# Kernel tuning notes

Hardware: AMD Instinct MI355X
Metric: run time of the kernel (lower is better)

## Reference

```python
import jax, jax.numpy as jnp
import numpy as np

B, S, D, E, TOP_K = 4, 4096, 2048, 64, 2

def setup_inputs() -> dict:
    key = jax.random.key(0)
    k1, k2, k3, k4 = jax.random.split(key, 4)
    return {
        "mh_output": jax.random.normal(k1, (B, S, D), dtype=jnp.float32),
        "W_route": jax.random.normal(k2, (D, E), dtype=jnp.float32) * (1.0 / np.sqrt(D)),
        "b_route": jnp.zeros((E,), dtype=jnp.float32),
        "W_noise": jax.random.normal(k3, (D, E), dtype=jnp.float32) * (1.0 / np.sqrt(D)),
        "b_noise": jnp.zeros((E,), dtype=jnp.float32),
        "noise": jax.random.normal(k4, (B, S, E), dtype=jnp.float32),
    }

def reference(mh_output, W_route, b_route, W_noise, b_noise, noise):
    # logits / noise logits: [B, S, E]
    logits = jnp.einsum("bsd,de->bse", mh_output, W_route) + b_route
    noise_logits = jnp.einsum("bsd,de->bse", mh_output, W_noise) + b_noise
    noisy_logits = logits + noise * jax.nn.softplus(noise_logits)

    top_vals, indices = jax.lax.top_k(noisy_logits, TOP_K)  # [B,S,K]

    # scatter top-k values into a -inf-filled tensor, then softmax
    flat_vals = top_vals.reshape(-1, TOP_K)
    flat_idx = indices.reshape(-1, TOP_K)
    n_tok = flat_idx.shape[0]
    rows = jnp.arange(n_tok)[:, None]
    sparse = jnp.full((n_tok, E), -jnp.inf, dtype=noisy_logits.dtype)
    sparse = sparse.at[rows, flat_idx].set(flat_vals)
    probs = jax.nn.softmax(sparse, axis=-1).reshape(noisy_logits.shape)
    return probs, indices
```

## Files before the change

kernel.cpp:

```cpp
#include <hip/hip_runtime.h>
#include <math.h>

#define M_TOK 16384
#define D_DIM 2048
#define E_EXP 64
#define BM    32
#define NT_H  16
#define FRAG_B 1040
#define TILE_B (12 * FRAG_B)
#define LL_LD 132
#define SMEM_BYTES (4 * TILE_B)

typedef float         f32x16 __attribute__((ext_vector_type(16)));
typedef short         bf16x8 __attribute__((ext_vector_type(8)));
typedef unsigned int  uint;

#define MFMA32(a, b, c) __builtin_amdgcn_mfma_f32_32x32x16_bf16((a), (b), (c), 0, 0, 0)

__device__ __forceinline__ unsigned short bfrne(float f) {
    unsigned int u = __float_as_uint(f);
    return (unsigned short)((u + 0x7fffu + ((u >> 16) & 1u)) >> 16);
}
__device__ __forceinline__ float bfhi(unsigned short h) {
    return __uint_as_float((unsigned int)h << 16);
}

__device__ __forceinline__ bool beats(float va, int ia, float vb, int ib) {
    return (va > vb) || (va == vb && ia < ib);
}

__device__ __forceinline__ void block_sync_lds() {
    asm volatile("s_waitcnt lgkmcnt(0)" ::: "memory");
    __builtin_amdgcn_s_barrier();
    asm volatile("" ::: "memory");
}

__global__ __launch_bounds__(256) void prep_w(
    const float* __restrict__ Wr, const float* __restrict__ Wn,
    unsigned short* __restrict__ Wg)
{
    const int g     = blockIdx.x * 256 + threadIdx.x;
    const int lane  = g & 63;
    const int ch    = (g >> 6) & 3;
    const int kstep = g >> 8;
    const int col   = ch * 32 + (lane & 31);
    const float* __restrict__ W = (col < 64) ? Wr : Wn;
    const int colL  = col & 63;
    const int kbase = kstep * 16 + (lane >> 5) * 8;

    bf16x8 o0, o1, o2;
    #pragma unroll
    for (int j = 0; j < 8; ++j) {
        const float w = W[(size_t)(kbase + j) * E_EXP + colL];
        const unsigned short h0 = bfrne(w);
        const float r  = w - bfhi(h0);
        const unsigned short h1 = bfrne(r);
        const float r2 = r - bfhi(h1);
        const unsigned short h2 = bfrne(r2);
        o0[j] = (short)h0; o1[j] = (short)h1; o2[j] = (short)h2;
    }
    #pragma unroll
    for (int p = 0; p < 3; ++p) {
        const size_t idx = (((size_t)kstep * 3 + p) * 4 + ch) * 64 + lane;
        const bf16x8 o = (p == 0) ? o0 : (p == 1) ? o1 : o2;
        *(bf16x8*)(Wg + idx * 8) = o;
    }
}

__device__ __forceinline__ void load_b_half(const unsigned short* __restrict__ Wg,
                                            int t, int s0, int wc, int lane,
                                            bf16x8 (&Bv)[2][3])
{
    #pragma unroll
    for (int s = 0; s < 2; ++s) {
        const int kstep = t * 4 + s0 + s;
        #pragma unroll
        for (int p = 0; p < 3; ++p) {
            const size_t idx = (((size_t)kstep * 3 + p) * 4 + wc);
            Bv[s][p] = *(const bf16x8*)(Wg + (idx << 9) + lane * 8);
        }
    }
}

__device__ __forceinline__ void load_a(const float* __restrict__ A, int tokBase,
                                       int t, int tid, float4& x)
{
    const int row = tid >> 4;
    const int kc  = tid & 15;
    x = *(const float4*)(A + (size_t)(tokBase + row) * D_DIM + t * 64 + kc * 4);
}

__device__ __forceinline__ void cvt_store(char* tbase, int tid, const float4& x)
{
    const float v[4] = {x.x, x.y, x.z, x.w};
    uint t0[4], t1[4]; unsigned short h2[4];
    #pragma unroll
    for (int j = 0; j < 4; ++j) {
        const uint u = __float_as_uint(v[j]);
        t0[j] = u & 0xffff0000u;
        const float r = v[j] - __uint_as_float(t0[j]);
        const uint ru = __float_as_uint(r);
        t1[j] = ru & 0xffff0000u;
        const float r2 = r - __uint_as_float(t1[j]);
        h2[j] = bfrne(r2);
    }
    uint2 w0, w1, w2;
    w0.x = (t0[0] >> 16) | t0[1];  w0.y = (t0[2] >> 16) | t0[3];
    w1.x = (t1[0] >> 16) | t1[1];  w1.y = (t1[2] >> 16) | t1[3];
    w2.x = (uint)h2[0] | ((uint)h2[1] << 16);
    w2.y = (uint)h2[2] | ((uint)h2[3] << 16);

    const int row   = tid >> 4;
    const int kc    = tid & 15;
    const int kstep = kc >> 2;
    const int hoct  = (kc >> 1) & 1;
    const int half  = kc & 1;
    const int l     = hoct * 32 + row;
    char* p = tbase + kstep * (3 * FRAG_B) + l * 16 + half * 8;
    *(uint2*)(p)              = w0;
    *(uint2*)(p + FRAG_B)     = w1;
    *(uint2*)(p + 2 * FRAG_B) = w2;
}

__device__ __forceinline__ void compute_half(const char* buf, int s0, int lane,
                                             const bf16x8 (&Bv)[2][3],
                                             f32x16& acch, f32x16& accl)
{
    const char* ap = buf + lane * 16;
    #pragma unroll
    for (int s = 0; s < 2; ++s) {
        const int f = (s0 + s) * 3;
        const bf16x8 a0 = *(const bf16x8*)(ap + (f + 0) * FRAG_B);
        const bf16x8 a1 = *(const bf16x8*)(ap + (f + 1) * FRAG_B);
        const bf16x8 a2 = *(const bf16x8*)(ap + (f + 2) * FRAG_B);
        acch = MFMA32(a0, Bv[s][0], acch);
        accl = MFMA32(a0, Bv[s][1], accl);
        accl = MFMA32(a1, Bv[s][0], accl);
        accl = MFMA32(a1, Bv[s][1], accl);
        accl = MFMA32(a0, Bv[s][2], accl);
        accl = MFMA32(a2, Bv[s][0], accl);
    }
}

__global__ __launch_bounds__(512, 4) void fused_router(
    const float* __restrict__ A,
    const unsigned short* __restrict__ Wg,
    const float* __restrict__ br, const float* __restrict__ bn,
    const float* __restrict__ noise,
    float* __restrict__ probs, float* __restrict__ idxo)
{
    __shared__ __align__(16) char smem[SMEM_BYTES];

    const int tid  = threadIdx.x;
    const int lane = tid & 63;
    const int wid  = tid >> 6;
    const int wc   = wid & 3;
    const int kh   = wid >> 2;
    const int tokBase = blockIdx.x * BM;

    f32x16 acch, accl;
    #pragma unroll
    for (int r = 0; r < 16; ++r) { acch[r] = 0.f; accl[r] = 0.f; }

    char* s0a = smem;
    char* s0b = smem + TILE_B;
    char* s1a = smem + 2 * TILE_B;
    char* s1b = smem + 3 * TILE_B;
    const char* myB0 = smem + (kh * 2 + 0) * TILE_B;
    const char* myB1 = smem + (kh * 2 + 1) * TILE_B;

    bf16x8 Bx[2][3], By[2][3];
    float4 x0, x1;

    load_a(A, tokBase, 0,        tid, x0);
    load_a(A, tokBase, NT_H,     tid, x1);
    cvt_store(s0a, tid, x0);
    cvt_store(s1a, tid, x1);
    load_a(A, tokBase, 1,        tid, x0);
    load_a(A, tokBase, NT_H + 1, tid, x1);
    load_b_half(Wg, kh * NT_H, 0, wc, lane, Bx);
    block_sync_lds();

    #pragma unroll 1
    for (int it = 0; it < NT_H; it += 2) {
        const int tA = kh * NT_H + it;

        cvt_store(s0b, tid, x0);
        cvt_store(s1b, tid, x1);
        if (it + 2 < NT_H) {
            load_a(A, tokBase, it + 2,        tid, x0);
            load_a(A, tokBase, NT_H + it + 2, tid, x1);
        }
        load_b_half(Wg, tA, 2, wc, lane, By);
        __builtin_amdgcn_s_setprio(1);
        compute_half(myB0, 0, lane, Bx, acch, accl);
        __builtin_amdgcn_s_setprio(0);
        load_b_half(Wg, tA + 1, 0, wc, lane, Bx);
        __builtin_amdgcn_s_setprio(1);
        compute_half(myB0, 2, lane, By, acch, accl);
        __builtin_amdgcn_s_setprio(0);
        block_sync_lds();

        if (it + 2 < NT_H) {
            cvt_store(s0a, tid, x0);
            cvt_store(s1a, tid, x1);
        }
        if (it + 3 < NT_H) {
            load_a(A, tokBase, it + 3,        tid, x0);
            load_a(A, tokBase, NT_H + it + 3, tid, x1);
        }
        load_b_half(Wg, tA + 1, 2, wc, lane, By);
        __builtin_amdgcn_s_setprio(1);
        compute_half(myB1, 0, lane, Bx, acch, accl);
        __builtin_amdgcn_s_setprio(0);
        if (it + 2 < NT_H) load_b_half(Wg, tA + 2, 0, wc, lane, Bx);
        __builtin_amdgcn_s_setprio(1);
        compute_half(myB1, 2, lane, By, acch, accl);
        __builtin_amdgcn_s_setprio(0);
        block_sync_lds();
    }

    float (*Ll)[BM][LL_LD] = (float (*)[BM][LL_LD])smem;
    {
        const int col   = wc * 32 + (lane & 31);
        const int rbase = 4 * (lane >> 5);
        #pragma unroll
        for (int r = 0; r < 16; ++r) {
            const int row = (r & 3) + 8 * (r >> 2) + rbase;
            Ll[kh][row][col] = acch[r] + accl[r];
        }
    }
    block_sync_lds();

    const int token = tid >> 4;
    const int s16   = tid & 15;
    const int tokG  = tokBase + token;

    float v0 = -INFINITY, v1 = -INFINITY;
    int i0 = 0, i1 = 0;
    {
        const float4 n4 = *(const float4*)(noise + (size_t)tokG * E_EXP + s16 * 4);
        const float4 b4 = *(const float4*)(br + s16 * 4);
        const float4 c4 = *(const float4*)(bn + s16 * 4);
        const float4 la = *(const float4*)(&Ll[0][token][s16 * 4]);
        const float4 lb = *(const float4*)(&Ll[1][token][s16 * 4]);
        const float4 ma = *(const float4*)(&Ll[0][token][64 + s16 * 4]);
        const float4 mb = *(const float4*)(&Ll[1][token][64 + s16 * 4]);
        const float nv[4] = {n4.x, n4.y, n4.z, n4.w};
        const float bv[4] = {b4.x, b4.y, b4.z, b4.w};
        const float cv[4] = {c4.x, c4.y, c4.z, c4.w};
        const float lv[4] = {la.x + lb.x, la.y + lb.y, la.z + lb.z, la.w + lb.w};
        const float mv[4] = {ma.x + mb.x, ma.y + mb.y, ma.z + mb.z, ma.w + mb.w};
        #pragma unroll
        for (int j = 0; j < 4; ++j) {
            const int e = s16 * 4 + j;
            const float lg = lv[j] + bv[j];
            const float nl = mv[j] + cv[j];
            const float sp = fmaxf(nl, 0.0f) + log1pf(expf(-fabsf(nl)));
            const float v  = fmaf(nv[j], sp, lg);
            if (beats(v, e, v0, i0))      { v1 = v0; i1 = i0; v0 = v; i0 = e; }
            else if (beats(v, e, v1, i1)) { v1 = v;  i1 = e; }
        }
    }
    #pragma unroll
    for (int m = 1; m < 16; m <<= 1) {
        const float w0 = __shfl_xor(v0, m), w1 = __shfl_xor(v1, m);
        const int   j0 = __shfl_xor(i0, m), j1 = __shfl_xor(i1, m);
        if (beats(v0, i0, w0, j0)) {
            if (!beats(v1, i1, w0, j0)) { v1 = w0; i1 = j0; }
        } else {
            if (beats(v0, i0, w1, j1)) { v1 = v0; i1 = i0; }
            else                       { v1 = w1; i1 = j1; }
            v0 = w0; i0 = j0;
        }
    }
    const float e1  = expf(v1 - v0);
    const float den = 1.0f + e1;
    const float p0 = 1.0f / den;
    const float p1 = e1 / den;

    float out[4];
    #pragma unroll
    for (int j = 0; j < 4; ++j) {
        const int e = s16 * 4 + j;
        out[j] = (e == i0) ? p0 : ((e == i1) ? p1 : 0.0f);
    }
    *(float4*)(probs + (size_t)tokG * E_EXP + s16 * 4) =
        make_float4(out[0], out[1], out[2], out[3]);
    if (s16 == 0)
        *(float2*)(idxo + (size_t)tokG * 2) = make_float2((float)i0, (float)i1);
}

extern "C" void kernel_launch(void* const* d_in, const int* in_sizes, int n_in,
                              void* d_out, int out_size, void* d_ws, size_t ws_size,
                              hipStream_t stream) {
    (void)in_sizes; (void)n_in; (void)out_size; (void)ws_size;
    const float* A  = (const float*)d_in[0];
    const float* Wr = (const float*)d_in[1];
    const float* br = (const float*)d_in[2];
    const float* Wn = (const float*)d_in[3];
    const float* bn = (const float*)d_in[4];
    const float* nz = (const float*)d_in[5];

    float* probs = (float*)d_out;
    float* idxo  = probs + (size_t)M_TOK * E_EXP;

    unsigned short* Wg = (unsigned short*)d_ws;

    prep_w<<<128, 256, 0, stream>>>(Wr, Wn, Wg);
    fused_router<<<M_TOK / BM, 512, 0, stream>>>(A, Wg, br, bn, nz, probs, idxo);
}
```

Before: 237.2 us.

## Restructure main loop into per-k-step phases with finer-grained barriers

Replaces the two-half-tile compute blocks with four per-k-step phases per tile. Each phase issues its LDS A reads and next-step B global loads, then meets a barrier and waits on lgkmcnt before a short MFMA burst under raised priority, followed by another barrier. The A conversion stores and prefetch are spread across the later phases to interleave memory and matrix work more evenly between waves. This adds many more barriers per tile, and the B register double-buffer shrinks to a single k-step. That cuts register pressure but leaves less latency slack for the global B loads.

```diff
diff --git a/kernel.cpp b/kernel.cpp
--- a/kernel.cpp
+++ b/kernel.cpp
@@ -29,12 +29,6 @@
     return (va > vb) || (va == vb && ia < ib);
 }
 
-__device__ __forceinline__ void block_sync_lds() {
-    asm volatile("s_waitcnt lgkmcnt(0)" ::: "memory");
-    __builtin_amdgcn_s_barrier();
-    asm volatile("" ::: "memory");
-}
-
 __global__ __launch_bounds__(256) void prep_w(
     const float* __restrict__ Wr, const float* __restrict__ Wn,
     unsigned short* __restrict__ Wg)
@@ -67,18 +61,13 @@
     }
 }
 
-__device__ __forceinline__ void load_b_half(const unsigned short* __restrict__ Wg,
-                                            int t, int s0, int wc, int lane,
-                                            bf16x8 (&Bv)[2][3])
-{
-    #pragma unroll
-    for (int s = 0; s < 2; ++s) {
-        const int kstep = t * 4 + s0 + s;
-        #pragma unroll
-        for (int p = 0; p < 3; ++p) {
-            const size_t idx = (((size_t)kstep * 3 + p) * 4 + wc);
-            Bv[s][p] = *(const bf16x8*)(Wg + (idx << 9) + lane * 8);
-        }
+__device__ __forceinline__ void load_b_k(const unsigned short* __restrict__ Wg,
+                                         int kstep, int wc, int lane, bf16x8 (&B)[3])
+{
+    #pragma unroll
+    for (int p = 0; p < 3; ++p) {
+        const size_t idx = ((size_t)(kstep * 3 + p) * 4 + wc);
+        B[p] = *(const bf16x8*)(Wg + (idx << 9) + lane * 8);
     }
 }
 
@@ -122,24 +111,41 @@
     *(uint2*)(p + 2 * FRAG_B) = w2;
 }
 
-__device__ __forceinline__ void compute_half(const char* buf, int s0, int lane,
-                                             const bf16x8 (&Bv)[2][3],
-                                             f32x16& acch, f32x16& accl)
-{
-    const char* ap = buf + lane * 16;
-    #pragma unroll
-    for (int s = 0; s < 2; ++s) {
-        const int f = (s0 + s) * 3;
-        const bf16x8 a0 = *(const bf16x8*)(ap + (f + 0) * FRAG_B);
-        const bf16x8 a1 = *(const bf16x8*)(ap + (f + 1) * FRAG_B);
-        const bf16x8 a2 = *(const bf16x8*)(ap + (f + 2) * FRAG_B);
-        acch = MFMA32(a0, Bv[s][0], acch);
-        accl = MFMA32(a0, Bv[s][1], accl);
-        accl = MFMA32(a1, Bv[s][0], accl);
-        accl = MFMA32(a1, Bv[s][1], accl);
-        accl = MFMA32(a0, Bv[s][2], accl);
-        accl = MFMA32(a2, Bv[s][0], accl);
-    }
+#define PHASE_BODY(P, BC, NK, BN, EXTRA) do {                        \
+    const char* ap_ = cbuf + (P) * (3 * FRAG_B) + lane * 16;         \
+    const bf16x8 a0_ = *(const bf16x8*)(ap_);                        \
+    const bf16x8 a1_ = *(const bf16x8*)(ap_ + FRAG_B);               \
+    const bf16x8 a2_ = *(const bf16x8*)(ap_ + 2 * FRAG_B);           \
+    load_b_k(Wg, (NK), wc, lane, BN);                                \
+    EXTRA                                                            \
+    __builtin_amdgcn_s_barrier();                                    \
+    asm volatile("s_waitcnt lgkmcnt(0)" ::: "memory");               \
+    __builtin_amdgcn_s_setprio(1);                                   \
+    acch = MFMA32(a0_, BC[0], acch);                                 \
+    accl = MFMA32(a0_, BC[1], accl);                                 \
+    accl = MFMA32(a1_, BC[0], accl);                                 \
+    accl = MFMA32(a1_, BC[1], accl);                                 \
+    accl = MFMA32(a0_, BC[2], accl);                                 \
+    accl = MFMA32(a2_, BC[0], accl);                                 \
+    __builtin_amdgcn_s_setprio(0);                                   \
+    __builtin_amdgcn_s_barrier();                                    \
+} while (0)
+
+__device__ __forceinline__ void run_tile(
+    const float* __restrict__ A, const unsigned short* __restrict__ Wg,
+    const char* cbuf, char* d0, char* d1, int t, bool do_cvt, bool do_lda,
+    int tokBase, int tid, int lane, int wc, int kh,
+    bf16x8 (&BX)[3], bf16x8 (&BY)[3],
+    float4& x0, float4& x1, f32x16& acch, f32x16& accl)
+{
+    const int kbase = (kh * NT_H + t) * 4;
+    PHASE_BODY(0, BX, kbase + 1, BY, );
+    PHASE_BODY(1, BY, kbase + 2, BX, );
+    PHASE_BODY(2, BX, kbase + 3, BY, if (do_cvt) cvt_store(d0, tid, x0); );
+    PHASE_BODY(3, BY, kbase + 4, BX,
+        if (do_cvt) cvt_store(d1, tid, x1);
+        if (do_lda) { load_a(A, tokBase, t + 2, tid, x0);
+                      load_a(A, tokBase, NT_H + t + 2, tid, x1); } );
 }
 
 __global__ __launch_bounds__(512, 4) void fused_router(
@@ -169,7 +175,7 @@
     const char* myB0 = smem + (kh * 2 + 0) * TILE_B;
     const char* myB1 = smem + (kh * 2 + 1) * TILE_B;
 
-    bf16x8 Bx[2][3], By[2][3];
+    bf16x8 BX[3], BY[3];
     float4 x0, x1;
 
     load_a(A, tokBase, 0,        tid, x0);
@@ -178,46 +184,17 @@
     cvt_store(s1a, tid, x1);
     load_a(A, tokBase, 1,        tid, x0);
     load_a(A, tokBase, NT_H + 1, tid, x1);
-    load_b_half(Wg, kh * NT_H, 0, wc, lane, Bx);
-    block_sync_lds();
+    load_b_k(Wg, (kh * NT_H) * 4, wc, lane, BX);
+    asm volatile("s_waitcnt lgkmcnt(0)" ::: "memory");
+    __builtin_amdgcn_s_barrier();
+    asm volatile("" ::: "memory");
 
     #pragma unroll 1
-    for (int it = 0; it < NT_H; it += 2) {
-        const int tA = kh * NT_H + it;
-
-        cvt_store(s0b, tid, x0);
-        cvt_store(s1b, tid, x1);
-        if (it + 2 < NT_H) {
-            load_a(A, tokBase, it + 2,        tid, x0);
-            load_a(A, tokBase, NT_H + it + 2, tid, x1);
-        }
-        load_b_half(Wg, tA, 2, wc, lane, By);
-        __builtin_amdgcn_s_setprio(1);
-        compute_half(myB0, 0, lane, Bx, acch, accl);
-        __builtin_amdgcn_s_setprio(0);
-        load_b_half(Wg, tA + 1, 0, wc, lane, Bx);
-        __builtin_amdgcn_s_setprio(1);
-        compute_half(myB0, 2, lane, By, acch, accl);
-        __builtin_amdgcn_s_setprio(0);
-        block_sync_lds();
-
-        if (it + 2 < NT_H) {
-            cvt_store(s0a, tid, x0);
-            cvt_store(s1a, tid, x1);
-        }
-        if (it + 3 < NT_H) {
-            load_a(A, tokBase, it + 3,        tid, x0);
-            load_a(A, tokBase, NT_H + it + 3, tid, x1);
-        }
-        load_b_half(Wg, tA + 1, 2, wc, lane, By);
-        __builtin_amdgcn_s_setprio(1);
-        compute_half(myB1, 0, lane, Bx, acch, accl);
-        __builtin_amdgcn_s_setprio(0);
-        if (it + 2 < NT_H) load_b_half(Wg, tA + 2, 0, wc, lane, Bx);
-        __builtin_amdgcn_s_setprio(1);
-        compute_half(myB1, 2, lane, By, acch, accl);
-        __builtin_amdgcn_s_setprio(0);
-        block_sync_lds();
+    for (int t = 0; t < NT_H; t += 2) {
+        run_tile(A, Wg, myB0, s0b, s1b, t, true, t + 2 < NT_H,
+                 tokBase, tid, lane, wc, kh, BX, BY, x0, x1, acch, accl);
+        run_tile(A, Wg, myB1, s0a, s1a, t + 1, t + 2 < NT_H, t + 3 < NT_H,
+                 tokBase, tid, lane, wc, kh, BX, BY, x0, x1, acch, accl);
     }
 
     float (*Ll)[BM][LL_LD] = (float (*)[BM][LL_LD])smem;
@@ -230,7 +207,9 @@
             Ll[kh][row][col] = acch[r] + accl[r];
         }
     }
-    block_sync_lds();
+    asm volatile("s_waitcnt lgkmcnt(0)" ::: "memory");
+    __builtin_amdgcn_s_barrier();
+    asm volatile("" ::: "memory");
 
     const int token = tid >> 4;
     const int s16   = tid & 15;
```

After: 226.3 us. 4.6% less time.
